# Kernel optimization log

Measured on AMD Instinct MI355X. Metric: run time of the kernel, lower is better.

Reference implementation:

```python
import jax, jax.numpy as jnp
import numpy as np

DIM = 384
HEADS = 6
NEG = -1e9  # masked-score fill; equivalent to gathering only kept K/V rows


def setup_inputs() -> dict:
    key = jax.random.key(0)
    ks = jax.random.split(key, 9)
    B, N, C = 1, 4098, DIM
    x = jax.random.normal(ks[0], (B, N, C), dtype=jnp.float32)
    pos = jax.random.normal(ks[1], (B, N + 1, C), dtype=jnp.float32)
    # float mask in [0,1); >=0.5 means 'foreground / keep as key', <0.5 pooled into back token
    mask = jax.random.uniform(ks[2], (B, 1, N - 2), dtype=jnp.float32)
    mask_block = jnp.ones((N + 1,), dtype=jnp.float32)  # positions 0, N-1, N always kept
    Wq = jax.random.normal(ks[3], (C, C), dtype=jnp.float32) * 0.02
    Wk = jax.random.normal(ks[4], (C, C), dtype=jnp.float32) * 0.02
    Wv = jax.random.normal(ks[5], (C, C), dtype=jnp.float32) * 0.02
    Wp = jax.random.normal(ks[6], (C, C), dtype=jnp.float32) * 0.02
    bp = jnp.zeros((C,), dtype=jnp.float32)
    return {"x": x, "pos": pos, "mask": mask, "mask_block": mask_block,
            "Wq": Wq, "Wk": Wk, "Wv": Wv, "Wp": Wp, "bp": bp}


def reference(x, pos, mask, mask_block, Wq, Wk, Wv, Wp, bp):
    B, N, C = x.shape
    H = HEADS
    D = C // H
    scale = D ** -0.5
    eps = 1e-10

    # back token: average of background (mask < 0.5) interior tokens
    reverse = jnp.where(mask < 0.5, 1.0, 0.0)                      # (B,1,N-2)
    pooled = jnp.einsum('bon,bnc->boc', reverse, x[:, 1:N - 1])    # (B,1,C)
    back_tokens = pooled / (reverse.sum(axis=2, keepdims=True) + eps)

    kv_x = jnp.concatenate([x, back_tokens], axis=1)               # (B,N+1,C)
    q_x = x + pos[:, :N]
    k_x = kv_x + pos

    q = (q_x @ Wq.T).reshape(B, N, H, D).transpose(0, 2, 1, 3)       # (B,H,N,D)
    k = (k_x @ Wk.T).reshape(B, N + 1, H, D).transpose(0, 2, 1, 3)   # (B,H,N+1,D)
    v = (kv_x @ Wv.T).reshape(B, N + 1, H, D).transpose(0, 2, 1, 3)  # (B,H,N+1,D)

    # key-selection mask: original gathers rows with mask_block >= 0.5;
    # masked softmax over all N+1 keys is mathematically identical.
    mb = mask_block.at[1:N - 1].set(mask[0, 0])
    keep = mb >= 0.5                                               # (N+1,)

    scores = jnp.einsum('bhqd,bhkd->bhqk', q, k) * scale
    scores = jnp.where(keep[None, None, None, :], scores, NEG)
    attn = jax.nn.softmax(scores, axis=-1)
    out = jnp.einsum('bhqk,bhkd->bhqd', attn, v)
    out = out.transpose(0, 2, 1, 3).reshape(B, N, C)
    return out @ Wp.T + bp
```

## Files before the change

kernel.cpp:

```cpp
#include <hip/hip_runtime.h>
#include <math.h>

#define N_TOK 4098
#define NK_TOK 4099
#define C_DIM 384
#define NKPAD 4160

typedef short  bh8 __attribute__((ext_vector_type(8)));
typedef float  f32x4 __attribute__((ext_vector_type(4)));
typedef unsigned short ushort;
typedef ushort u4 __attribute__((ext_vector_type(4)));
typedef ushort u8 __attribute__((ext_vector_type(8)));

static __device__ __forceinline__ ushort f2bf(float f) {
  unsigned int u = __float_as_uint(f);
  u = (u + 0x7FFF + ((u >> 16) & 1)) >> 16;
  return (ushort)u;
}
static __device__ __forceinline__ float bf2f(ushort s) {
  return __uint_as_float(((unsigned int)s) << 16);
}

__global__ __launch_bounds__(256) void prep_kernel(
    const float* __restrict__ x, const float* __restrict__ pos,
    const float* __restrict__ mask, const float* __restrict__ mask_block,
    const float* __restrict__ Wq, const float* __restrict__ Wk,
    const float* __restrict__ Wv, const float* __restrict__ Wp,
    float* __restrict__ pooled_part, float* __restrict__ cnt_part,
    int* __restrict__ nk, int* __restrict__ inv,
    ushort* __restrict__ Ak, ushort* __restrict__ Av, ushort* __restrict__ Wb) {
  const int b = blockIdx.x, t = threadIdx.x;
  if (b < 128) {
    const int r0 = b * 32;
    float a0 = 0.f, a1 = 0.f;
    int lc = 0;
    for (int r = r0; r < r0 + 32; ++r) {
      if (mask[r] < 0.5f) {
        a0 += x[(size_t)(r + 1) * C_DIM + t];
        if (t < 128) a1 += x[(size_t)(r + 1) * C_DIM + 256 + t];
        ++lc;
      }
    }
    pooled_part[b * C_DIM + t] = a0;
    if (t < 128) pooled_part[b * C_DIM + 256 + t] = a1;
    if (t == 0) cnt_part[b] = (float)lc;
  } else if (b == 128) {
    __shared__ int scnt[256];
    const int j0 = t * 17;
    unsigned int bits = 0;
    int c = 0;
#pragma unroll 1
    for (int u = 0; u < 17; ++u) {
      const int j = j0 + u;
      bool keep = false;
      if (j < NK_TOK)
        keep = (j >= 1 && j <= N_TOK - 2) ? (mask[j - 1] >= 0.5f)
                                          : (mask_block[j] >= 0.5f);
      if (keep) { bits |= 1u << u; ++c; }
    }
    scnt[t] = c;
    __syncthreads();
    for (int d = 1; d < 256; d <<= 1) {
      const int v = scnt[t];
      const int add = (t >= d) ? scnt[t - d] : 0;
      __syncthreads();
      scnt[t] = v + add;
      __syncthreads();
    }
    int base = scnt[t] - c;
    if (t == 255) *nk = scnt[255];
#pragma unroll 1
    for (int u = 0; u < 17; ++u) {
      const int j = j0 + u;
      if (j < NK_TOK) inv[j] = ((bits >> u) & 1) ? base++ : -1;
    }
  } else if (b < 258) {
    const int r0 = (b - 129) * 32;
#pragma unroll 3
    for (int i = 0; i < 12; ++i) {
      const int idx = i * 1024 + t * 4;
      const int row = r0 + idx / C_DIM, col = idx % C_DIM;
      if (row >= N_TOK) continue;
      const float4 pv = *(const float4*)&pos[(size_t)row * C_DIM + col];
      const float4 xv = *(const float4*)&x[(size_t)row * C_DIM + col];
      u4 k4 = {f2bf(xv.x + pv.x), f2bf(xv.y + pv.y),
               f2bf(xv.z + pv.z), f2bf(xv.w + pv.w)};
      *(u4*)&Ak[(size_t)row * C_DIM + col] = k4;
      u4 v4 = {f2bf(xv.x), f2bf(xv.y), f2bf(xv.z), f2bf(xv.w)};
      *(u4*)&Av[(size_t)row * C_DIM + col] = v4;
    }
  } else {
    const int wi = b - 258;
    const float* src = (wi < 8) ? Wq : (wi < 16) ? Wk : (wi < 24) ? Wv : Wp;
    const int base = (wi >> 3) * 147456 + (wi & 7) * 18432;
#pragma unroll 2
    for (int i = 0; i < 18; ++i) {
      const float4 v = *(const float4*)&src[(wi & 7) * 18432 + i * 1024 + t * 4];
      u4 o = {f2bf(v.x), f2bf(v.y), f2bf(v.z), f2bf(v.w)};
      *(u4*)&Wb[base + i * 1024 + t * 4] = o;
    }
  }
}

static __device__ __forceinline__ void gemm_core(
    const ushort* __restrict__ A, const ushort* __restrict__ B,
    ushort (* __restrict__ As)[72], ushort (* __restrict__ Bs)[72],
    int t, int w, int quad, int l15, f32x4 acc[4]) {
  const int g = t & 7;
  u8 ra[2], rb[2];
#pragma unroll
  for (int it = 0; it < 2; ++it) {
    const int r = it * 32 + (t >> 3);
    ra[it] = *(const u8*)&A[r * C_DIM + g * 8];
    rb[it] = *(const u8*)&B[r * C_DIM + g * 8];
  }
#pragma unroll 1
  for (int kt = 0; kt < 6; ++kt) {
    __syncthreads();
#pragma unroll
    for (int it = 0; it < 2; ++it) {
      const int r = it * 32 + (t >> 3);
      *(u8*)&As[r][g * 8] = ra[it];
      *(u8*)&Bs[r][g * 8] = rb[it];
    }
    __syncthreads();
    if (kt < 5) {
      const int k0 = (kt + 1) * 64;
#pragma unroll
      for (int it = 0; it < 2; ++it) {
        const int r = it * 32 + (t >> 3);
        ra[it] = *(const u8*)&A[r * C_DIM + k0 + g * 8];
        rb[it] = *(const u8*)&B[r * C_DIM + k0 + g * 8];
      }
    }
    const bh8 b0 = *(const bh8*)&Bs[w * 16 + l15][quad * 8];
    const bh8 b1 = *(const bh8*)&Bs[w * 16 + l15][32 + quad * 8];
#pragma unroll
    for (int mb = 0; mb < 4; ++mb) {
      const bh8 a0 = *(const bh8*)&As[mb * 16 + l15][quad * 8];
      const bh8 a1 = *(const bh8*)&As[mb * 16 + l15][32 + quad * 8];
      acc[mb] = __builtin_amdgcn_mfma_f32_16x16x32_bf16(a0, b0, acc[mb], 0, 0, 0);
      acc[mb] = __builtin_amdgcn_mfma_f32_16x16x32_bf16(a1, b1, acc[mb], 0, 0, 0);
    }
  }
}

__global__ __launch_bounds__(256) void gemm3_kernel(
    const ushort* __restrict__ Ak, const ushort* __restrict__ Av,
    const ushort* __restrict__ Wb, const int* __restrict__ inv,
    const float* __restrict__ pooled_part, const float* __restrict__ cnt_part,
    const float* __restrict__ pos, ushort* __restrict__ Qh,
    ushort* __restrict__ Kc, ushort* __restrict__ Vt) {
  __shared__ ushort As[64][72], Bs[64][72];
  __shared__ float skin[C_DIM], svin[C_DIM];
  const int t = threadIdx.x, w = t >> 6, lane = t & 63;
  const int quad = lane >> 4, l15 = lane & 15;
  const int which = blockIdx.y / 6, h = blockIdx.y % 6;

  if (blockIdx.x == 65) {
    if (blockIdx.y != 0) return;
    float cs = 0.f;
    for (int i = 0; i < 128; ++i) cs += cnt_part[i];
    const float ic = 1.f / (cs + 1e-10f);
    for (int c = t; c < C_DIM; c += 256) {
      float s = 0.f;
      for (int p = 0; p < 128; ++p) s += pooled_part[p * C_DIM + c];
      const float back = s * ic;
      skin[c] = bf2f(f2bf(back + pos[(size_t)(NK_TOK - 1) * C_DIM + c]));
      svin[c] = bf2f(f2bf(back));
    }
    __syncthreads();
    const int slot = inv[NK_TOK - 1];
    for (int o = t; o < C_DIM; o += 256) {
      const ushort* wk = Wb + 147456 + (size_t)o * C_DIM;
      const ushort* wv = Wb + 294912 + (size_t)o * C_DIM;
      float ka = 0.f, va = 0.f;
#pragma unroll 4
      for (int c8 = 0; c8 < 48; ++c8) {
        const u8 k8 = *(const u8*)&wk[c8 * 8];
        const u8 v8 = *(const u8*)&wv[c8 * 8];
#pragma unroll
        for (int j = 0; j < 8; ++j) {
          ka += bf2f(k8[j]) * skin[c8 * 8 + j];
          va += bf2f(v8[j]) * svin[c8 * 8 + j];
        }
      }
      const int hh = o >> 6, d = o & 63;
      Kc[((size_t)hh * NKPAD + slot) * 64 + d] = f2bf(ka);
      Vt[((size_t)(hh * 64 + d)) * NKPAD + slot] = f2bf(va);
    }
    return;
  }

  const int m0 = blockIdx.x * 64;
  const ushort* A = (which == 2 ? Av : Ak) + (size_t)m0 * C_DIM;
  const ushort* B = Wb + (size_t)which * 147456 + (size_t)h * 64 * C_DIM;
  f32x4 acc[4];
#pragma unroll
  for (int i = 0; i < 4; ++i) acc[i] = (f32x4){0.f, 0.f, 0.f, 0.f};
  gemm_core(A, B, As, Bs, t, w, quad, l15, acc);
  const int n = w * 16 + l15;
  if (which == 0) {
#pragma unroll
    for (int mb = 0; mb < 4; ++mb)
#pragma unroll
      for (int r = 0; r < 4; ++r) {
        const int m = m0 + mb * 16 + quad * 4 + r;
        if (m < N_TOK)
          Qh[((size_t)h * N_TOK + m) * 64 + n] = f2bf(acc[mb][r] * 0.125f);
      }
  } else if (which == 1) {
#pragma unroll
    for (int mb = 0; mb < 4; ++mb)
#pragma unroll
      for (int r = 0; r < 4; ++r) {
        const int m = m0 + mb * 16 + quad * 4 + r;
        if (m < NK_TOK - 1) {
          const int slot = inv[m];
          if (slot >= 0) Kc[((size_t)h * NKPAD + slot) * 64 + n] = f2bf(acc[mb][r]);
        }
      }
  } else {
#pragma unroll
    for (int mb = 0; mb < 4; ++mb)
#pragma unroll
      for (int r = 0; r < 4; ++r) {
        const int m = m0 + mb * 16 + quad * 4 + r;
        if (m < NK_TOK - 1) {
          const int slot = inv[m];
          if (slot >= 0) Vt[((size_t)(h * 64 + n)) * NKPAD + slot] = f2bf(acc[mb][r]);
        }
      }
  }
}

__global__ __launch_bounds__(256) void attn_kernel(
    const ushort* __restrict__ Qh, const ushort* __restrict__ Kc,
    const ushort* __restrict__ Vt, const int* __restrict__ nkp,
    ushort* __restrict__ Opart, float* __restrict__ Lpart) {
  __shared__ ushort Ks[64][72];
  __shared__ ushort Vs[64][72];
  __shared__ ushort Ps[4][32][72];
  const int t = threadIdx.x, w = t >> 6, lane = t & 63;
  const int quad = lane >> 4, l15 = lane & 15;
  const int h = blockIdx.y, slice = blockIdx.z;
  const int q0 = blockIdx.x * 128;
  const int nk = *nkp, nchunk = (nk + 63) >> 6;
  const int g8 = t & 7;

  bh8 qf[2][2];
#pragma unroll
  for (int g = 0; g < 2; ++g) {
    int qr = q0 + w * 32 + g * 16 + l15;
    if (qr > N_TOK - 1) qr = N_TOK - 1;
    const ushort* qp = Qh + ((size_t)h * N_TOK + qr) * 64 + quad * 8;
    qf[g][0] = *(const bh8*)qp;
    qf[g][1] = *(const bh8*)(qp + 32);
  }
  f32x4 oacc[2][4];
#pragma unroll
  for (int g = 0; g < 2; ++g)
#pragma unroll
    for (int i = 0; i < 4; ++i) oacc[g][i] = (f32x4){0.f, 0.f, 0.f, 0.f};
  float l_r[2] = {0.f, 0.f};

  const ushort* kb = Kc + (size_t)h * NKPAD * 64;
  const ushort* vb = Vt + (size_t)h * 64 * NKPAD;

  u8 rk[2], rv[2];
  if (slice < nchunk) {
#pragma unroll
    for (int it = 0; it < 2; ++it) {
      const int r = it * 32 + (t >> 3);
      rk[it] = *(const u8*)&kb[(size_t)(slice * 64 + r) * 64 + g8 * 8];
      rv[it] = *(const u8*)&vb[(size_t)r * NKPAD + slice * 64 + g8 * 8];
    }
  }
#pragma unroll 1
  for (int kc = slice; kc < nchunk; kc += 3) {
    __syncthreads();
#pragma unroll
    for (int it = 0; it < 2; ++it) {
      const int r = it * 32 + (t >> 3);
      *(u8*)&Ks[r][g8 * 8] = rk[it];
      *(u8*)&Vs[r][g8 * 8] = rv[it];
    }
    __syncthreads();
    if (kc + 3 < nchunk) {
#pragma unroll
      for (int it = 0; it < 2; ++it) {
        const int r = it * 32 + (t >> 3);
        rk[it] = *(const u8*)&kb[(size_t)((kc + 3) * 64 + r) * 64 + g8 * 8];
        rv[it] = *(const u8*)&vb[(size_t)r * NKPAD + (kc + 3) * 64 + g8 * 8];
      }
    }
    float csum[2] = {0.f, 0.f};
#pragma unroll
    for (int f = 0; f < 4; ++f) {
      const bh8 a0 = *(const bh8*)&Ks[f * 16 + l15][quad * 8];
      const bh8 a1 = *(const bh8*)&Ks[f * 16 + l15][32 + quad * 8];
      const int keyb = kc * 64 + f * 16 + quad * 4;
#pragma unroll
      for (int g = 0; g < 2; ++g) {
        f32x4 s4 = {0.f, 0.f, 0.f, 0.f};
        s4 = __builtin_amdgcn_mfma_f32_16x16x32_bf16(a0, qf[g][0], s4, 0, 0, 0);
        s4 = __builtin_amdgcn_mfma_f32_16x16x32_bf16(a1, qf[g][1], s4, 0, 0, 0);
        u4 pv;
#pragma unroll
        for (int r = 0; r < 4; ++r) {
          const float p = (keyb + r < nk) ? __expf(s4[r]) : 0.f;
          csum[g] += p;
          pv[r] = f2bf(p);
        }
        *(u4*)&Ps[w][g * 16 + l15][f * 16 + quad * 4] = pv;
      }
    }
#pragma unroll
    for (int g = 0; g < 2; ++g) {
      csum[g] += __shfl_xor(csum[g], 16);
      csum[g] += __shfl_xor(csum[g], 32);
      l_r[g] += csum[g];
    }
    bh8 pa[2][2];
#pragma unroll
    for (int g = 0; g < 2; ++g) {
      pa[g][0] = *(const bh8*)&Ps[w][g * 16 + l15][quad * 8];
      pa[g][1] = *(const bh8*)&Ps[w][g * 16 + l15][32 + quad * 8];
    }
#pragma unroll
    for (int db = 0; db < 4; ++db) {
      const bh8 b0 = *(const bh8*)&Vs[db * 16 + l15][quad * 8];
      const bh8 b1 = *(const bh8*)&Vs[db * 16 + l15][32 + quad * 8];
#pragma unroll
      for (int g = 0; g < 2; ++g) {
        oacc[g][db] = __builtin_amdgcn_mfma_f32_16x16x32_bf16(pa[g][0], b0, oacc[g][db], 0, 0, 0);
        oacc[g][db] = __builtin_amdgcn_mfma_f32_16x16x32_bf16(pa[g][1], b1, oacc[g][db], 0, 0, 0);
      }
    }
  }

  const int sh = slice * 6 + h;
#pragma unroll
  for (int g = 0; g < 2; ++g) {
#pragma unroll
    for (int db = 0; db < 4; ++db)
#pragma unroll
      for (int r = 0; r < 4; ++r) {
        const int q = q0 + w * 32 + g * 16 + quad * 4 + r;
        if (q < N_TOK)
          Opart[((size_t)sh * NKPAD + q) * 64 + db * 16 + l15] = f2bf(oacc[g][db][r]);
      }
    if (quad == 0) {
      const int q = q0 + w * 32 + g * 16 + l15;
      if (q < N_TOK) Lpart[sh * NKPAD + q] = l_r[g];
    }
  }
}

__global__ __launch_bounds__(256) void gemm_out_kernel(
    const ushort* __restrict__ Opart, const float* __restrict__ Lpart,
    const ushort* __restrict__ Wpb, const float* __restrict__ bp,
    float* __restrict__ out) {
  __shared__ ushort As[64][72], Bs[64][72];
  const int t = threadIdx.x, w = t >> 6, lane = t & 63;
  const int quad = lane >> 4, l15 = lane & 15;
  const int m0 = blockIdx.x * 64;
  const int n0 = blockIdx.y * 64;
  const int g8 = t & 7;
  f32x4 acc[4];
#pragma unroll
  for (int i = 0; i < 4; ++i) acc[i] = (f32x4){0.f, 0.f, 0.f, 0.f};

  u8 ra[2], rb[2];
#pragma unroll
  for (int it = 0; it < 2; ++it) {
    const int r = it * 32 + (t >> 3), m = m0 + r;
    float l = 0.f;
#pragma unroll
    for (int s = 0; s < 3; ++s) l += Lpart[(s * 6 + 0) * NKPAD + m];
    const float invl = 1.f / l;
    float o[8] = {0, 0, 0, 0, 0, 0, 0, 0};
#pragma unroll
    for (int s = 0; s < 3; ++s) {
      const u8 v = *(const u8*)&Opart[((size_t)(s * 6 + 0) * NKPAD + m) * 64 + g8 * 8];
#pragma unroll
      for (int j = 0; j < 8; ++j) o[j] += bf2f(v[j]);
    }
#pragma unroll
    for (int j = 0; j < 8; ++j) ra[it][j] = f2bf(o[j] * invl);
    rb[it] = *(const u8*)&Wpb[(size_t)(n0 + r) * C_DIM + g8 * 8];
  }
#pragma unroll 1
  for (int kt = 0; kt < 6; ++kt) {
    __syncthreads();
#pragma unroll
    for (int it = 0; it < 2; ++it) {
      const int r = it * 32 + (t >> 3);
      *(u8*)&As[r][g8 * 8] = ra[it];
      *(u8*)&Bs[r][g8 * 8] = rb[it];
    }
    __syncthreads();
    if (kt < 5) {
      const int kh = kt + 1;
#pragma unroll
      for (int it = 0; it < 2; ++it) {
        const int r = it * 32 + (t >> 3), m = m0 + r;
        float l = 0.f;
#pragma unroll
        for (int s = 0; s < 3; ++s) l += Lpart[(s * 6 + kh) * NKPAD + m];
        const float invl = 1.f / l;
        float o[8] = {0, 0, 0, 0, 0, 0, 0, 0};
#pragma unroll
        for (int s = 0; s < 3; ++s) {
          const u8 v = *(const u8*)&Opart[((size_t)(s * 6 + kh) * NKPAD + m) * 64 + g8 * 8];
#pragma unroll
          for (int j = 0; j < 8; ++j) o[j] += bf2f(v[j]);
        }
#pragma unroll
        for (int j = 0; j < 8; ++j) ra[it][j] = f2bf(o[j] * invl);
        rb[it] = *(const u8*)&Wpb[(size_t)(n0 + r) * C_DIM + kh * 64 + g8 * 8];
      }
    }
    const bh8 b0 = *(const bh8*)&Bs[w * 16 + l15][quad * 8];
    const bh8 b1 = *(const bh8*)&Bs[w * 16 + l15][32 + quad * 8];
#pragma unroll
    for (int mb = 0; mb < 4; ++mb) {
      const bh8 a0 = *(const bh8*)&As[mb * 16 + l15][quad * 8];
      const bh8 a1 = *(const bh8*)&As[mb * 16 + l15][32 + quad * 8];
      acc[mb] = __builtin_amdgcn_mfma_f32_16x16x32_bf16(a0, b0, acc[mb], 0, 0, 0);
      acc[mb] = __builtin_amdgcn_mfma_f32_16x16x32_bf16(a1, b1, acc[mb], 0, 0, 0);
    }
  }
  const int n = w * 16 + l15;
  const float bb = bp[n0 + n];
#pragma unroll
  for (int mb = 0; mb < 4; ++mb)
#pragma unroll
    for (int r = 0; r < 4; ++r) {
      const int m = m0 + mb * 16 + quad * 4 + r;
      if (m < N_TOK) out[(size_t)m * C_DIM + n0 + n] = acc[mb][r] + bb;
    }
}

extern "C" void kernel_launch(void* const* d_in, const int* in_sizes, int n_in,
                              void* d_out, int out_size, void* d_ws, size_t ws_size,
                              hipStream_t stream) {
  const float* x          = (const float*)d_in[0];
  const float* pos        = (const float*)d_in[1];
  const float* mask       = (const float*)d_in[2];
  const float* mask_block = (const float*)d_in[3];
  const float* Wq         = (const float*)d_in[4];
  const float* Wk         = (const float*)d_in[5];
  const float* Wv         = (const float*)d_in[6];
  const float* Wp         = (const float*)d_in[7];
  const float* bp         = (const float*)d_in[8];
  float* out = (float*)d_out;
  char* wsb = (char*)d_ws;

  float*  cnt_part    = (float*)wsb;
  int*    nk          = (int*)(wsb + 512);
  int*    inv         = (int*)(wsb + 1024);
  float*  pooled_part = (float*)(wsb + 20480);
  ushort* Ak          = (ushort*)(wsb + 217088);
  ushort* Av          = (ushort*)(wsb + 3411968);
  ushort* Wb          = (ushort*)(wsb + 6606848);
  ushort* Qh          = (ushort*)(wsb + 7786496);
  ushort* Kc          = (ushort*)(wsb + 10933760);
  ushort* Vt          = (ushort*)(wsb + 14128640);
  ushort* Op          = (ushort*)(wsb + 17323520);
  float*  Lp          = (float*)(wsb + 26908160);

  prep_kernel<<<dim3(290), dim3(256), 0, stream>>>(
      x, pos, mask, mask_block, Wq, Wk, Wv, Wp,
      pooled_part, cnt_part, nk, inv, Ak, Av, Wb);
  gemm3_kernel<<<dim3(66, 18), dim3(256), 0, stream>>>(
      Ak, Av, Wb, inv, pooled_part, cnt_part, pos, Qh, Kc, Vt);
  attn_kernel<<<dim3(33, 6, 3), dim3(256), 0, stream>>>(Qh, Kc, Vt, nk, Op, Lp);
  gemm_out_kernel<<<dim3(65, 6), dim3(256), 0, stream>>>(Op, Lp, Wb + 3 * 147456,
                                                         bp, out);
}
```

Baseline: 166.8 us.

## Halve attention query tile per block and coarsen background pooling partials

The attention kernel now gives each wave 16 query rows instead of 32, so a block covers 64 queries and the grid doubles to 65x6x3 blocks. The goal is more blocks across the CUs and fewer accumulator registers per wave. The cost is that each K/V chunk loaded into shared memory is reused by half as many queries. The background-token pooling in the prep kernel also moves from 128 blocks of 32 rows to 16 blocks of 256 rows, so the final reduction in gemm3 has fewer partials to sum but each pooling block takes longer.

Result: slower. 190.3 us (+14.1%).

```diff
diff --git a/kernel.cpp b/kernel.cpp
--- a/kernel.cpp
+++ b/kernel.cpp
@@ -30,11 +30,12 @@
     int* __restrict__ nk, int* __restrict__ inv,
     ushort* __restrict__ Ak, ushort* __restrict__ Av, ushort* __restrict__ Wb) {
   const int b = blockIdx.x, t = threadIdx.x;
-  if (b < 128) {
-    const int r0 = b * 32;
+  if (b < 16) {
+    const int r0 = b * 256;
     float a0 = 0.f, a1 = 0.f;
     int lc = 0;
-    for (int r = r0; r < r0 + 32; ++r) {
+#pragma unroll 4
+    for (int r = r0; r < r0 + 256; ++r) {
       if (mask[r] < 0.5f) {
         a0 += x[(size_t)(r + 1) * C_DIM + t];
         if (t < 128) a1 += x[(size_t)(r + 1) * C_DIM + 256 + t];
@@ -44,7 +45,7 @@
     pooled_part[b * C_DIM + t] = a0;
     if (t < 128) pooled_part[b * C_DIM + 256 + t] = a1;
     if (t == 0) cnt_part[b] = (float)lc;
-  } else if (b == 128) {
+  } else if (b == 16) {
     __shared__ int scnt[256];
     const int j0 = t * 17;
     unsigned int bits = 0;
@@ -74,8 +75,8 @@
       const int j = j0 + u;
       if (j < NK_TOK) inv[j] = ((bits >> u) & 1) ? base++ : -1;
     }
-  } else if (b < 258) {
-    const int r0 = (b - 129) * 32;
+  } else if (b < 146) {
+    const int r0 = (b - 17) * 32;
 #pragma unroll 3
     for (int i = 0; i < 12; ++i) {
       const int idx = i * 1024 + t * 4;
@@ -90,7 +91,7 @@
       *(u4*)&Av[(size_t)row * C_DIM + col] = v4;
     }
   } else {
-    const int wi = b - 258;
+    const int wi = b - 146;
     const float* src = (wi < 8) ? Wq : (wi < 16) ? Wk : (wi < 24) ? Wv : Wp;
     const int base = (wi >> 3) * 147456 + (wi & 7) * 18432;
 #pragma unroll 2
@@ -160,11 +161,13 @@
   if (blockIdx.x == 65) {
     if (blockIdx.y != 0) return;
     float cs = 0.f;
-    for (int i = 0; i < 128; ++i) cs += cnt_part[i];
+#pragma unroll
+    for (int i = 0; i < 16; ++i) cs += cnt_part[i];
     const float ic = 1.f / (cs + 1e-10f);
     for (int c = t; c < C_DIM; c += 256) {
       float s = 0.f;
-      for (int p = 0; p < 128; ++p) s += pooled_part[p * C_DIM + c];
+#pragma unroll
+      for (int p = 0; p < 16; ++p) s += pooled_part[p * C_DIM + c];
       const float back = s * ic;
       skin[c] = bf2f(f2bf(back + pos[(size_t)(NK_TOK - 1) * C_DIM + c]));
       svin[c] = bf2f(f2bf(back));
@@ -240,29 +243,26 @@
     ushort* __restrict__ Opart, float* __restrict__ Lpart) {
   __shared__ ushort Ks[64][72];
   __shared__ ushort Vs[64][72];
-  __shared__ ushort Ps[4][32][72];
+  __shared__ ushort Ps[4][16][72];
   const int t = threadIdx.x, w = t >> 6, lane = t & 63;
   const int quad = lane >> 4, l15 = lane & 15;
   const int h = blockIdx.y, slice = blockIdx.z;
-  const int q0 = blockIdx.x * 128;
+  const int q0 = blockIdx.x * 64;
   const int nk = *nkp, nchunk = (nk + 63) >> 6;
-  const int g8 = t & 7;
-
-  bh8 qf[2][2];
-#pragma unroll
-  for (int g = 0; g < 2; ++g) {
-    int qr = q0 + w * 32 + g * 16 + l15;
+  const int g = t & 7;
+
+  bh8 qf0, qf1;
+  {
+    int qr = q0 + w * 16 + l15;
     if (qr > N_TOK - 1) qr = N_TOK - 1;
     const ushort* qp = Qh + ((size_t)h * N_TOK + qr) * 64 + quad * 8;
-    qf[g][0] = *(const bh8*)qp;
-    qf[g][1] = *(const bh8*)(qp + 32);
-  }
-  f32x4 oacc[2][4];
-#pragma unroll
-  for (int g = 0; g < 2; ++g)
-#pragma unroll
-    for (int i = 0; i < 4; ++i) oacc[g][i] = (f32x4){0.f, 0.f, 0.f, 0.f};
-  float l_r[2] = {0.f, 0.f};
+    qf0 = *(const bh8*)qp;
+    qf1 = *(const bh8*)(qp + 32);
+  }
+  f32x4 oacc[4];
+#pragma unroll
+  for (int i = 0; i < 4; ++i) oacc[i] = (f32x4){0.f, 0.f, 0.f, 0.f};
+  float l_r = 0.f;
 
   const ushort* kb = Kc + (size_t)h * NKPAD * 64;
   const ushort* vb = Vt + (size_t)h * 64 * NKPAD;
@@ -272,8 +272,8 @@
 #pragma unroll
     for (int it = 0; it < 2; ++it) {
       const int r = it * 32 + (t >> 3);
-      rk[it] = *(const u8*)&kb[(size_t)(slice * 64 + r) * 64 + g8 * 8];
-      rv[it] = *(const u8*)&vb[(size_t)r * NKPAD + slice * 64 + g8 * 8];
+      rk[it] = *(const u8*)&kb[(size_t)(slice * 64 + r) * 64 + g * 8];
+      rv[it] = *(const u8*)&vb[(size_t)r * NKPAD + slice * 64 + g * 8];
     }
   }
 #pragma unroll 1
@@ -282,78 +282,64 @@
 #pragma unroll
     for (int it = 0; it < 2; ++it) {
       const int r = it * 32 + (t >> 3);
-      *(u8*)&Ks[r][g8 * 8] = rk[it];
-      *(u8*)&Vs[r][g8 * 8] = rv[it];
+      *(u8*)&Ks[r][g * 8] = rk[it];
+      *(u8*)&Vs[r][g * 8] = rv[it];
     }
     __syncthreads();
     if (kc + 3 < nchunk) {
 #pragma unroll
       for (int it = 0; it < 2; ++it) {
         const int r = it * 32 + (t >> 3);
-        rk[it] = *(const u8*)&kb[(size_t)((kc + 3) * 64 + r) * 64 + g8 * 8];
-        rv[it] = *(const u8*)&vb[(size_t)r * NKPAD + (kc + 3) * 64 + g8 * 8];
-      }
-    }
-    float csum[2] = {0.f, 0.f};
+        rk[it] = *(const u8*)&kb[(size_t)((kc + 3) * 64 + r) * 64 + g * 8];
+        rv[it] = *(const u8*)&vb[(size_t)r * NKPAD + (kc + 3) * 64 + g * 8];
+      }
+    }
+    float csum = 0.f;
 #pragma unroll
     for (int f = 0; f < 4; ++f) {
+      f32x4 s4 = {0.f, 0.f, 0.f, 0.f};
       const bh8 a0 = *(const bh8*)&Ks[f * 16 + l15][quad * 8];
       const bh8 a1 = *(const bh8*)&Ks[f * 16 + l15][32 + quad * 8];
+      s4 = __builtin_amdgcn_mfma_f32_16x16x32_bf16(a0, qf0, s4, 0, 0, 0);
+      s4 = __builtin_amdgcn_mfma_f32_16x16x32_bf16(a1, qf1, s4, 0, 0, 0);
       const int keyb = kc * 64 + f * 16 + quad * 4;
-#pragma unroll
-      for (int g = 0; g < 2; ++g) {
-        f32x4 s4 = {0.f, 0.f, 0.f, 0.f};
-        s4 = __builtin_amdgcn_mfma_f32_16x16x32_bf16(a0, qf[g][0], s4, 0, 0, 0);
-        s4 = __builtin_amdgcn_mfma_f32_16x16x32_bf16(a1, qf[g][1], s4, 0, 0, 0);
-        u4 pv;
-#pragma unroll
-        for (int r = 0; r < 4; ++r) {
-          const float p = (keyb + r < nk) ? __expf(s4[r]) : 0.f;
-          csum[g] += p;
-          pv[r] = f2bf(p);
-        }
-        *(u4*)&Ps[w][g * 16 + l15][f * 16 + quad * 4] = pv;
-      }
-    }
-#pragma unroll
-    for (int g = 0; g < 2; ++g) {
-      csum[g] += __shfl_xor(csum[g], 16);
-      csum[g] += __shfl_xor(csum[g], 32);
-      l_r[g] += csum[g];
-    }
-    bh8 pa[2][2];
-#pragma unroll
-    for (int g = 0; g < 2; ++g) {
-      pa[g][0] = *(const bh8*)&Ps[w][g * 16 + l15][quad * 8];
-      pa[g][1] = *(const bh8*)&Ps[w][g * 16 + l15][32 + quad * 8];
-    }
+      u4 pv;
+#pragma unroll
+      for (int r = 0; r < 4; ++r) {
+        const float p = (keyb + r < nk) ? __expf(s4[r]) : 0.f;
+        csum += p;
+        pv[r] = f2bf(p);
+      }
+      *(u4*)&Ps[w][l15][f * 16 + quad * 4] = pv;
+    }
+    csum += __shfl_xor(csum, 16);
+    csum += __shfl_xor(csum, 32);
+    l_r += csum;
+
+    const bh8 pa0 = *(const bh8*)&Ps[w][l15][quad * 8];
+    const bh8 pa1 = *(const bh8*)&Ps[w][l15][32 + quad * 8];
 #pragma unroll
     for (int db = 0; db < 4; ++db) {
       const bh8 b0 = *(const bh8*)&Vs[db * 16 + l15][quad * 8];
       const bh8 b1 = *(const bh8*)&Vs[db * 16 + l15][32 + quad * 8];
-#pragma unroll
-      for (int g = 0; g < 2; ++g) {
-        oacc[g][db] = __builtin_amdgcn_mfma_f32_16x16x32_bf16(pa[g][0], b0, oacc[g][db], 0, 0, 0);
-        oacc[g][db] = __builtin_amdgcn_mfma_f32_16x16x32_bf16(pa[g][1], b1, oacc[g][db], 0, 0, 0);
-      }
+      oacc[db] = __builtin_amdgcn_mfma_f32_16x16x32_bf16(pa0, b0, oacc[db], 0, 0, 0);
+      oacc[db] = __builtin_amdgcn_mfma_f32_16x16x32_bf16(pa1, b1, oacc[db], 0, 0, 0);
     }
   }
 
   const int sh = slice * 6 + h;
-#pragma unroll
-  for (int g = 0; g < 2; ++g) {
-#pragma unroll
-    for (int db = 0; db < 4; ++db)
-#pragma unroll
-      for (int r = 0; r < 4; ++r) {
-        const int q = q0 + w * 32 + g * 16 + quad * 4 + r;
-        if (q < N_TOK)
-          Opart[((size_t)sh * NKPAD + q) * 64 + db * 16 + l15] = f2bf(oacc[g][db][r]);
-      }
-    if (quad == 0) {
-      const int q = q0 + w * 32 + g * 16 + l15;
-      if (q < N_TOK) Lpart[sh * NKPAD + q] = l_r[g];
-    }
+  const int qg = q0 + w * 16;
+#pragma unroll
+  for (int db = 0; db < 4; ++db)
+#pragma unroll
+    for (int r = 0; r < 4; ++r) {
+      const int q = qg + quad * 4 + r;
+      if (q < N_TOK)
+        Opart[((size_t)sh * NKPAD + q) * 64 + db * 16 + l15] = f2bf(oacc[db][r]);
+    }
+  if (quad == 0) {
+    const int q = qg + l15;
+    if (q < N_TOK) Lpart[sh * NKPAD + q] = l_r;
   }
 }
 
@@ -470,12 +456,12 @@
   ushort* Op          = (ushort*)(wsb + 17323520);
   float*  Lp          = (float*)(wsb + 26908160);
 
-  prep_kernel<<<dim3(290), dim3(256), 0, stream>>>(
+  prep_kernel<<<dim3(178), dim3(256), 0, stream>>>(
       x, pos, mask, mask_block, Wq, Wk, Wv, Wp,
       pooled_part, cnt_part, nk, inv, Ak, Av, Wb);
   gemm3_kernel<<<dim3(66, 18), dim3(256), 0, stream>>>(
       Ak, Av, Wb, inv, pooled_part, cnt_part, pos, Qh, Kc, Vt);
-  attn_kernel<<<dim3(33, 6, 3), dim3(256), 0, stream>>>(Qh, Kc, Vt, nk, Op, Lp);
+  attn_kernel<<<dim3(65, 6, 3), dim3(256), 0, stream>>>(Qh, Kc, Vt, nk, Op, Lp);
   gemm_out_kernel<<<dim3(65, 6), dim3(256), 0, stream>>>(Op, Lp, Wb + 3 * 147456,
                                                          bp, out);
 }
```
